# Kernel tuning notes

Measured on AMD Instinct MI355X. Metric: run time of the kernel, lower is better.

## Reference

```python
import jax, jax.numpy as jnp
import numpy as np

B, T, G, M, D = 8, 2048, 2, 1024, 256
ALPHA = -1.0      # config['dist_to_logits_alpha']
TAU = 2.0         # curr_temp = max_temp at init
EPS = 1e-10


def setup_inputs() -> dict:
    key = jax.random.key(0)
    k1, k2, k3 = jax.random.split(key, 3)
    x = jax.random.normal(k1, (B, T, G * D), dtype=jnp.float32)
    # nn.init.uniform_(embedding, -0.999, 0.999)
    embedding = jax.random.uniform(k2, (G, M, D), dtype=jnp.float32, minval=-0.999, maxval=0.999)
    # uniform noise for gumbel sampling, clipped away from {0,1}
    gumbel_u = jax.random.uniform(k3, (B * T, G, M), dtype=jnp.float32, minval=1e-6, maxval=1.0 - 1e-6)
    return {"x": x, "embedding": embedding, "gumbel_u": gumbel_u}


def reference(x, embedding, gumbel_u):
    b, t, c = x.shape
    g, m, d = embedding.shape
    xf = x.reshape(-1, g, d)                                  # [N, G, D]

    sq_e = jnp.sum(embedding ** 2, axis=-1)                   # [G, M]
    sq_x = jnp.sum(xf ** 2, axis=-1, keepdims=True)           # [N, G, 1]
    cross = jnp.einsum('ngd,gmd->ngm', xf, embedding)         # [N, G, M]
    logits = ALPHA * (sq_e[None] + sq_x - 2.0 * cross)        # [N, G, M]

    # hard-assignment code perplexity
    hard_x = jax.nn.one_hot(jnp.argmax(logits, axis=-1), m, dtype=logits.dtype)
    hard_probs = hard_x.mean(axis=0)                          # [G, M]
    code_perplexity = -jnp.sum(hard_probs * jnp.log2(hard_probs + EPS), axis=-1)

    # soft-assignment prob perplexity
    avg_probs = jax.nn.softmax(logits, axis=-1).mean(axis=0)  # [G, M]
    prob_perplexity = -jnp.sum(avg_probs * jnp.log2(avg_probs + EPS), axis=-1)

    # gumbel-softmax (hard=True, straight-through)
    gumbels = -jnp.log(-jnp.log(gumbel_u))
    y_soft = jax.nn.softmax((logits + gumbels) / TAU, axis=-1)
    idx = jnp.argmax(y_soft, axis=-1)                         # [N, G]
    y_hard = jax.nn.one_hot(idx, m, dtype=y_soft.dtype)
    st = y_hard + y_soft - jax.lax.stop_gradient(y_soft)      # straight-through one-hot

    # weighted sum over the codebook (avoids [N, G, M, D] blowup of the original)
    quantized = jnp.einsum('ngm,gmd->ngd', st, embedding).reshape(b, t, c)

    quantization_inds = idx.reshape(b, t, g).astype(jnp.int32)
    # use_vq_loss=True: F.mse_loss(x, quantized.detach())
    commitment_loss = jnp.mean((x - jax.lax.stop_gradient(quantized)) ** 2)

    return quantized, code_perplexity, prob_perplexity, quantization_inds, commitment_loss
```

## Files before the change

### kernel.cpp

```cpp
#include <hip/hip_runtime.h>
#include <math.h>

#define NTOT 16384
#define GG 2
#define MM 1024
#define DD 256

#define OFF_Q  ((size_t)0)
#define OFF_CP ((size_t)8388608)
#define OFF_PP ((size_t)8388610)
#define OFF_I  ((size_t)8388612)
#define OFF_L  ((size_t)8421380)

#define SHIFT 40.0f
#define REFINE_GAP 0.03f

typedef __attribute__((ext_vector_type(8))) short bf16x8;
typedef __attribute__((ext_vector_type(4))) float f32x4;
typedef unsigned short u16;
typedef unsigned int u32;

__device__ inline float wave_sum_f(float v) {
#pragma unroll
  for (int o = 32; o > 0; o >>= 1) v += __shfl_xor(v, o);
  return v;
}
__device__ inline u16 f2bf(float f) {
  u32 u = __float_as_uint(f);
  return (u16)((u + 0x7fffu + ((u >> 16) & 1u)) >> 16);
}
__device__ inline float bf2f(u16 h) {
  return __uint_as_float(((u32)h) << 16);
}
__device__ inline void async16(const void* g, void* l) {
  __builtin_amdgcn_global_load_lds(
      (const __attribute__((address_space(1))) u32*)g,
      (__attribute__((address_space(3))) u32*)l, 16, 0, 0);
}
__device__ inline float neg_log_acc(float u) {
  float t1 = 1.0f - u;
  float se = t1 * (1.f + t1 * (0.5f + t1 * (0.33333334f + t1 * 0.25f)));
  float fl = -__logf(u);
  return (t1 < 0.015625f) ? se : fl;
}

#define WS_INVZ   32768
#define WS_EHSW   163840
#define WS_ELSW   1212416
#define WS_EST    2260992
#define WS_NEED3  (2260992ull + 2ull * MM * (size_t)NTOT * GG)

__global__ void vq_init2(const float* __restrict__ emb, float* __restrict__ sq_e,
                         float* __restrict__ avg, int* __restrict__ hist,
                         double* __restrict__ loss, u16* __restrict__ eh,
                         u16* __restrict__ el, int do_split) {
  const int row = blockIdx.x * 4 + (threadIdx.x >> 6);
  const int lane = threadIdx.x & 63;
  float4 e4 = *(const float4*)&emb[(size_t)row * DD + lane * 4];
  float s = e4.x * e4.x + e4.y * e4.y + e4.z * e4.z + e4.w * e4.w;
  s = wave_sum_f(s);
  if (do_split) {
    ushort4 h, l;
    h.x = f2bf(e4.x); l.x = f2bf(e4.x - bf2f(h.x));
    h.y = f2bf(e4.y); l.y = f2bf(e4.y - bf2f(h.y));
    h.z = f2bf(e4.z); l.z = f2bf(e4.z - bf2f(h.z));
    h.w = f2bf(e4.w); l.w = f2bf(e4.w - bf2f(h.w));
    *(ushort4*)&eh[(size_t)row * DD + lane * 4] = h;
    *(ushort4*)&el[(size_t)row * DD + lane * 4] = l;
  }
  if (lane == 0) sq_e[row] = s;
  if (blockIdx.x == 0) {
    for (int i = threadIdx.x; i < GG * MM; i += 256) { avg[i] = 0.f; hist[i] = 0; }
    if (threadIdx.x == 0) *loss = 0.0;
  }
}

__global__ void vq_init_swz(const float* __restrict__ emb, u16* __restrict__ eh_sw,
                            u16* __restrict__ el_sw) {
  int tid = blockIdx.x * 256 + threadIdx.x;
  int g = tid >> 15, rem = tid & 32767;
  int col = rem >> 5, kc = rem & 31;
  const float* src = emb + ((size_t)(g * MM + col)) * DD + kc * 8;
  float4 fa = *(const float4*)src;
  float4 fb = *(const float4*)(src + 4);
  float f[8] = {fa.x, fa.y, fa.z, fa.w, fb.x, fb.y, fb.z, fb.w};
  u16 hi[8], lo[8];
#pragma unroll
  for (int j = 0; j < 8; ++j) {
    hi[j] = f2bf(f[j]);
    lo[j] = f2bf(f[j] - bf2f(hi[j]));
  }
  int ct = col >> 6, cg = (col >> 4) & 3, l15 = col & 15;
  int ks = kc >> 2, quad = kc & 3;
  size_t chunk = ((((size_t)g * 16 + ct) * 8 + ks) * 4 + cg) * 64 + quad * 16 + l15;
  ushort4* dh = (ushort4*)(eh_sw + chunk * 8);
  ushort4* dl = (ushort4*)(el_sw + chunk * 8);
  dh[0] = make_ushort4(hi[0], hi[1], hi[2], hi[3]);
  dh[1] = make_ushort4(hi[4], hi[5], hi[6], hi[7]);
  dl[0] = make_ushort4(lo[0], lo[1], lo[2], lo[3]);
  dl[1] = make_ushort4(lo[4], lo[5], lo[6], lo[7]);
}

__global__ __launch_bounds__(512, 2) void vq_main3(
    const float* __restrict__ x, const float* __restrict__ emb,
    const float* __restrict__ gum, const float* __restrict__ sq_e,
    const u16* __restrict__ eh_sw, const u16* __restrict__ el_sw,
    float* __restrict__ out, u16* __restrict__ est, float* __restrict__ invZ_ws,
    int* __restrict__ hist, double* __restrict__ loss) {
  __shared__ u16 bt[2][32768];
  __shared__ int fidx_lds[128];

  const int g = blockIdx.y;
  const int n0 = blockIdx.x * 128;
  const int t = threadIdx.x;
  const int wave = t >> 6, lane = t & 63;
  const int quad = lane >> 4, l15 = lane & 15;
  const int nw = n0 + wave * 16;

  float* xs = (float*)&bt[0][0];
  {
    const float* xb = x + (size_t)nw * (GG * DD) + (size_t)g * DD;
#pragma unroll 4
    for (int j = 0; j < 16; ++j) {
      float4 v = *(const float4*)(xb + (size_t)j * (GG * DD) + lane * 4);
      *(float4*)&xs[wave * 4096 + j * 256 + ((lane ^ (j & 7)) << 2)] = v;
    }
  }

  bf16x8 ah[8], al[8];
#pragma unroll
  for (int ks = 0; ks < 8; ++ks) {
    int row = l15;
    int c0 = ks * 8 + quad * 2;
    const float* base = &xs[wave * 4096 + row * 256];
    float4 f0 = *(const float4*)&base[((c0 ^ (row & 7)) << 2)];
    float4 f1 = *(const float4*)&base[(((c0 + 1) ^ (row & 7)) << 2)];
    float f[8] = {f0.x, f0.y, f0.z, f0.w, f1.x, f1.y, f1.z, f1.w};
#pragma unroll
    for (int j = 0; j < 8; ++j) {
      u16 h = f2bf(f[j]);
      ah[ks][j] = (short)h;
      al[ks][j] = (short)f2bf(f[j] - bf2f(h));
    }
  }
  __syncthreads();

  const u16* sgh = eh_sw + (size_t)g * 16 * 16384;
  const u16* sgl = el_sw + (size_t)g * 16 * 16384;

  auto stage = [&](int ct, int buf) {
    const u16* sh = sgh + (size_t)ct * 16384;
    const u16* sl = sgl + (size_t)ct * 16384;
    u16* dh = &bt[buf][0];
    u16* dl = &bt[buf][16384];
#pragma unroll
    for (int j = 0; j < 4; ++j) {
      int slot = j * 8 + wave;
      async16(sh + slot * 512 + lane * 8, dh + slot * 512);
      async16(sl + slot * 512 + lane * 8, dl + slot * 512);
    }
  };

  float Zl[4], hv[4], z1[4], z2[4];
  int hid[4], i1[4], i2[4];
#pragma unroll
  for (int i = 0; i < 4; ++i) {
    Zl[i] = 0.f; hv[i] = -INFINITY; z1[i] = -INFINITY; z2[i] = -INFINITY;
    hid[i] = 0; i1[i] = 0; i2[i] = 0;
  }

  stage(0, 0);

  const float* gumb = gum + ((size_t)(nw + quad * 4) * GG + g) * MM + l15;
  const float* sqb = sq_e + g * MM + l15;
  float gA[4], gB[4], sqA, sqB;
#pragma unroll
  for (int r = 0; r < 4; ++r) gA[r] = gumb[(size_t)r * (GG * MM)];
#pragma unroll
  for (int r = 0; r < 4; ++r) gB[r] = gumb[(size_t)r * (GG * MM) + 16];
  sqA = sqb[0];
  sqB = sqb[16];

#pragma unroll 1
  for (int ct = 0; ct < 16; ++ct) {
    __syncthreads();
    if (ct < 15) stage(ct + 1, (ct + 1) & 1);
    const u16* bh_p = &bt[ct & 1][0];
    const u16* bl_p = &bt[ct & 1][16384];
#pragma unroll 1
    for (int cg = 0; cg < 4; ++cg) {
      const int s = ct * 4 + cg;
      const int colG = s * 16 + l15;
      int sn = s + 2; if (sn > 63) sn = 63;
      float gN[4], sqN;
#pragma unroll
      for (int r = 0; r < 4; ++r) gN[r] = gumb[(size_t)r * (GG * MM) + sn * 16];
      sqN = sqb[sn * 16];

      f32x4 c0 = {0,0,0,0}, c1 = {0,0,0,0}, c2 = {0,0,0,0};
#pragma unroll
      for (int ks = 0; ks < 8; ++ks) {
        int off = ((ks * 4 + cg) * 64 + lane) * 8;
        bf16x8 bh = *(const bf16x8*)(bh_p + off);
        bf16x8 bl = *(const bf16x8*)(bl_p + off);
        c0 = __builtin_amdgcn_mfma_f32_16x16x32_bf16(ah[ks], bh, c0, 0, 0, 0);
        c1 = __builtin_amdgcn_mfma_f32_16x16x32_bf16(ah[ks], bl, c1, 0, 0, 0);
        c2 = __builtin_amdgcn_mfma_f32_16x16x32_bf16(al[ks], bh, c2, 0, 0, 0);
      }
      float ev[4];
#pragma unroll
      for (int r = 0; r < 4; ++r) {
        float lp = 2.f * (c0[r] + c1[r] + c2[r]) - sqA + SHIFT;
        float e = __expf(fminf(lp, 80.f));
        Zl[r] += e;
        ev[r] = e;
        if (lp > hv[r]) { hv[r] = lp; hid[r] = colG; }
        float zz = lp - __logf(neg_log_acc(gA[r]));
        if (zz > z1[r]) {
          z2[r] = z1[r]; i2[r] = i1[r];
          z1[r] = zz; i1[r] = colG;
        } else if (zz > z2[r]) {
          z2[r] = zz; i2[r] = colG;
        }
      }
      u32 p01, p23;
      asm("v_cvt_pk_bf16_f32 %0, %1, %2" : "=v"(p01) : "v"(ev[0]), "v"(ev[1]));
      asm("v_cvt_pk_bf16_f32 %0, %1, %2" : "=v"(p23) : "v"(ev[2]), "v"(ev[3]));
      uint2 pk2 = make_uint2(p01, p23);
      *(uint2*)&est[((size_t)(g * MM + colG) << 14) + nw + quad * 4] = pk2;
#pragma unroll
      for (int r = 0; r < 4; ++r) { gA[r] = gB[r]; gB[r] = gN[r]; }
      sqA = sqB; sqB = sqN;
    }
  }

#pragma unroll 1
  for (int r = 0; r < 4; ++r) {
    const int row = wave * 16 + quad * 4 + r;
    const int n = n0 + row;
    float Zr = Zl[r], hvr = hv[r];
    int hir = hid[r];
    float v1 = z1[r], v2 = z2[r];
    int j1 = i1[r], j2 = i2[r];
#pragma unroll
    for (int o = 1; o <= 8; o <<= 1) {
      Zr += __shfl_xor(Zr, o);
      float ohv = __shfl_xor(hvr, o); int ohi = __shfl_xor(hir, o);
      if (ohv > hvr || (ohv == hvr && ohi < hir)) { hvr = ohv; hir = ohi; }
      float w1 = __shfl_xor(v1, o), w2 = __shfl_xor(v2, o);
      int k1 = __shfl_xor(j1, o), k2 = __shfl_xor(j2, o);
      if (w1 > v1 || (w1 == v1 && k1 < j1)) {
        if (v1 > w2 || (v1 == w2 && j1 < k2)) { v2 = v1; j2 = j1; }
        else { v2 = w2; j2 = k2; }
        v1 = w1; j1 = k1;
      } else if (w1 > v2 || (w1 == v2 && k1 < j2)) { v2 = w1; j2 = k1; }
    }
    int fidx = j1;
    if (v1 - v2 < REFINE_GAP) {
      const float* xrow = x + (size_t)n * (GG * DD) + (size_t)g * DD;
      const float* eA = emb + ((size_t)g * MM + j1) * DD;
      const float* eB = emb + ((size_t)g * MM + j2) * DD;
      double dA = 0, sA = 0, dB = 0, sB = 0;
#pragma unroll
      for (int k = 0; k < 16; ++k) {
        int d = l15 * 16 + k;
        double xv = (double)xrow[d];
        double ea = (double)eA[d], eb = (double)eB[d];
        dA += xv * ea; sA += ea * ea;
        dB += xv * eb; sB += eb * eb;
      }
#pragma unroll
      for (int o = 1; o <= 8; o <<= 1) {
        dA += __shfl_xor(dA, o); sA += __shfl_xor(sA, o);
        dB += __shfl_xor(dB, o); sB += __shfl_xor(sB, o);
      }
      double uA = (double)gum[((size_t)n * GG + g) * MM + j1];
      double uB = (double)gum[((size_t)n * GG + g) * MM + j2];
      double zA = 2.0 * dA - sA - log(-log(uA));
      double zB = 2.0 * dB - sB - log(-log(uB));
      if (zB > zA || (zB == zA && j2 < j1)) fidx = j2;
    }
    if (l15 == 0) {
      out[OFF_I + (size_t)n * GG + g] = (float)fidx;
      atomicAdd(&hist[g * MM + hir], 1);
      invZ_ws[g * NTOT + n] = 1.f / Zr;
      fidx_lds[row] = fidx;
    }
  }
  __syncthreads();

  {
    float ls = 0.f;
#pragma unroll
    for (int j = 0; j < 16; ++j) {
      int idx = j * 512 + t;
      int row = idx >> 6, f4 = idx & 63;
      int n = n0 + row, fi = fidx_lds[row];
      float4 e4 = *(const float4*)&emb[((size_t)g * MM + fi) * DD + f4 * 4];
      float4 x4 = *(const float4*)&x[(size_t)n * (GG * DD) + (size_t)g * DD + f4 * 4];
      *(float4*)&out[OFF_Q + (size_t)n * (GG * DD) + (size_t)g * DD + f4 * 4] = e4;
      float dx = x4.x - e4.x, dy = x4.y - e4.y, dz = x4.z - e4.z, dw = x4.w - e4.w;
      ls += dx * dx + dy * dy + dz * dz + dw * dw;
    }
    ls = wave_sum_f(ls);
    if (lane == 0) atomicAdd(loss, (double)ls);
  }
}

__global__ void vq_avg(const u16* __restrict__ est, const float* __restrict__ invZ,
                       float* __restrict__ avg) {
  int wid = blockIdx.x;
  int t = threadIdx.x;
  const u16* base = est + ((size_t)wid << 14);
  const float* zp = invZ + ((wid >> 10) << 14);
  float acc = 0.f;
#pragma unroll
  for (int it = 0; it < 8; ++it) {
    int n = it * 2048 + t * 8;
    uint4 e = *(const uint4*)(base + n);
    float4 z0 = *(const float4*)(zp + n);
    float4 z1 = *(const float4*)(zp + n + 4);
    acc += bf2f((u16)(e.x & 0xffff)) * z0.x + bf2f((u16)(e.x >> 16)) * z0.y +
           bf2f((u16)(e.y & 0xffff)) * z0.z + bf2f((u16)(e.y >> 16)) * z0.w +
           bf2f((u16)(e.z & 0xffff)) * z1.x + bf2f((u16)(e.z >> 16)) * z1.y +
           bf2f((u16)(e.w & 0xffff)) * z1.z + bf2f((u16)(e.w >> 16)) * z1.w;
  }
  acc = wave_sum_f(acc);
  __shared__ float sw[4];
  if ((t & 63) == 0) sw[t >> 6] = acc;
  __syncthreads();
  if (t == 0) avg[wid] = sw[0] + sw[1] + sw[2] + sw[3];
}

__global__ void vq_fin(const float* __restrict__ avg, const int* __restrict__ hist,
                       const double* __restrict__ loss, float* __restrict__ out) {
  int g = blockIdx.x, t = threadIdx.x;
  float cp = 0.f, pp = 0.f;
  for (int m = t; m < MM; m += 256) {
    float hp = (float)hist[g * MM + m] * (1.f / 16384.f);
    cp += hp * log2f(hp + 1e-10f);
    float ap = avg[g * MM + m] * (1.f / 16384.f);
    pp += ap * log2f(ap + 1e-10f);
  }
  cp = wave_sum_f(cp);
  pp = wave_sum_f(pp);
  __shared__ float sc[4], sp[4];
  int wave = t >> 6, lane = t & 63;
  if (lane == 0) { sc[wave] = cp; sp[wave] = pp; }
  __syncthreads();
  if (t == 0) {
    out[OFF_CP + g] = -(sc[0] + sc[1] + sc[2] + sc[3]);
    out[OFF_PP + g] = -(sp[0] + sp[1] + sp[2] + sp[3]);
    if (g == 0) out[OFF_L] = (float)(*loss * (1.0 / 8388608.0));
  }
}

__global__ __launch_bounds__(256, 3) void vq_main_fast(
    const float* __restrict__ x, const float* __restrict__ emb,
    const float* __restrict__ gum, const float* __restrict__ sq_e,
    const u16* __restrict__ eh, const u16* __restrict__ el,
    float* __restrict__ out, float* __restrict__ avg,
    int* __restrict__ hist, double* __restrict__ loss) {
  __shared__ u16 est_lds[4][16][264];
  __shared__ float colsum[MM];
  __shared__ float red[16][4][8];
  __shared__ float fin_invZ[16];
  __shared__ int fin_idx[16];

  const int g = blockIdx.y;
  const int n0 = blockIdx.x * 16;
  const int t = threadIdx.x;
  const int wave = t >> 6, lane = t & 63;
  const int quad = lane >> 4, l15 = lane & 15;
  const int wm0 = wave * 256;

  for (int i = t; i < MM; i += 256) colsum[i] = 0.f;

  bf16x8 ah[8], al[8];
  {
    const float* xr = x + (size_t)(n0 + l15) * (GG * DD) + (size_t)g * DD + quad * 8;
#pragma unroll
    for (int ks = 0; ks < 8; ++ks) {
      float4 fa = *(const float4*)(xr + ks * 32);
      float4 fb = *(const float4*)(xr + ks * 32 + 4);
      float f[8] = {fa.x, fa.y, fa.z, fa.w, fb.x, fb.y, fb.z, fb.w};
#pragma unroll
      for (int j = 0; j < 8; ++j) {
        u16 h = f2bf(f[j]);
        ah[ks][j] = (short)h;
        al[ks][j] = (short)f2bf(f[j] - bf2f(h));
      }
    }
  }
  const u16* ehb = eh + ((size_t)g * MM + wm0 + l15) * DD + quad * 8;
  const u16* elb = el + ((size_t)g * MM + wm0 + l15) * DD + quad * 8;
  const float* sqb = sq_e + g * MM + wm0 + l15;

  float Z[4] = {0.f, 0.f, 0.f, 0.f};
  float hv[4] = {-INFINITY, -INFINITY, -INFINITY, -INFINITY};
  int hid[4] = {0, 0, 0, 0};
  float z1[4] = {-INFINITY, -INFINITY, -INFINITY, -INFINITY};
  float z2[4] = {-INFINITY, -INFINITY, -INFINITY, -INFINITY};
  int i1[4] = {0, 0, 0, 0}, i2[4] = {0, 0, 0, 0};

#pragma unroll 2
  for (int tt = 0; tt < 16; ++tt) {
    float sqv = sqb[tt * 16];
    float gv[4];
#pragma unroll
    for (int r = 0; r < 4; ++r)
      gv[r] = gum[((size_t)(n0 + quad * 4 + r) * GG + g) * MM + wm0 + tt * 16 + l15];
    f32x4 a0 = {0,0,0,0}, a1 = {0,0,0,0}, a2 = {0,0,0,0};
#pragma unroll
    for (int ks = 0; ks < 8; ++ks) {
      bf16x8 bh = *(const bf16x8*)(ehb + (size_t)tt * 16 * DD + ks * 32);
      bf16x8 bl = *(const bf16x8*)(elb + (size_t)tt * 16 * DD + ks * 32);
      a0 = __builtin_amdgcn_mfma_f32_16x16x32_bf16(ah[ks], bh, a0, 0, 0, 0);
      a1 = __builtin_amdgcn_mfma_f32_16x16x32_bf16(ah[ks], bl, a1, 0, 0, 0);
      a2 = __builtin_amdgcn_mfma_f32_16x16x32_bf16(al[ks], bh, a2, 0, 0, 0);
    }
    const int colL = tt * 16 + l15;
    const int colG = wm0 + colL;
#pragma unroll
    for (int r = 0; r < 4; ++r) {
      float lp = 2.f * (a0[r] + a1[r] + a2[r]) - sqv + SHIFT;
      float ev = expf(fminf(lp, 80.f));
      Z[r] += ev;
      est_lds[wave][quad * 4 + r][colL] = f2bf(ev);
      if (lp > hv[r]) { hv[r] = lp; hid[r] = colG; }
      float zz = lp - logf(-logf(gv[r]));
      if (zz > z1[r]) { z2[r] = z1[r]; i2[r] = i1[r]; z1[r] = zz; i1[r] = colG; }
      else if (zz > z2[r]) { z2[r] = zz; i2[r] = colG; }
    }
  }
#pragma unroll
  for (int r = 0; r < 4; ++r) {
    float Zr = Z[r], hvr = hv[r];
    int hir = hid[r];
    float v1 = z1[r], v2 = z2[r];
    int j1 = i1[r], j2 = i2[r];
#pragma unroll
    for (int o = 1; o <= 8; o <<= 1) {
      Zr += __shfl_xor(Zr, o);
      float ohv = __shfl_xor(hvr, o); int ohi = __shfl_xor(hir, o);
      if (ohv > hvr || (ohv == hvr && ohi < hir)) { hvr = ohv; hir = ohi; }
      float w1 = __shfl_xor(v1, o), w2 = __shfl_xor(v2, o);
      int k1 = __shfl_xor(j1, o), k2 = __shfl_xor(j2, o);
      if (w1 > v1 || (w1 == v1 && k1 < j1)) {
        if (v1 > w2 || (v1 == w2 && j1 < k2)) { v2 = v1; j2 = j1; }
        else { v2 = w2; j2 = k2; }
        v1 = w1; j1 = k1;
      } else if (w1 > v2 || (w1 == v2 && k1 < j2)) { v2 = w1; j2 = k1; }
    }
    if (l15 == 0) {
      float* rp = red[quad * 4 + r][wave];
      rp[0] = Zr; rp[1] = hvr; rp[2] = __int_as_float(hir);
      rp[3] = v1; rp[4] = __int_as_float(j1);
      rp[5] = v2; rp[6] = __int_as_float(j2);
    }
  }
  __syncthreads();
  if (t < 16) {
    const int row = t, n = n0 + row;
    float Zf = 0.f, hvf = -INFINITY; int hif = 0;
    float v1 = -INFINITY, v2 = -INFINITY; int j1 = 0, j2 = 0;
    for (int w = 0; w < 4; ++w) {
      const float* rp = red[row][w];
      Zf += rp[0];
      float ohv = rp[1]; int ohi = __float_as_int(rp[2]);
      if (ohv > hvf || (ohv == hvf && ohi < hif)) { hvf = ohv; hif = ohi; }
      float w1 = rp[3], w2 = rp[5];
      int k1 = __float_as_int(rp[4]), k2 = __float_as_int(rp[6]);
      if (w1 > v1 || (w1 == v1 && k1 < j1)) {
        if (v1 > w2 || (v1 == w2 && j1 < k2)) { v2 = v1; j2 = j1; }
        else { v2 = w2; j2 = k2; }
        v1 = w1; j1 = k1;
      } else if (w1 > v2 || (w1 == v2 && k1 < j2)) { v2 = w1; j2 = k1; }
    }
    int fidx = j1;
    if (v1 - v2 < REFINE_GAP) {
      const float* xrow = x + (size_t)n * (GG * DD) + (size_t)g * DD;
      const float* eA = emb + ((size_t)g * MM + j1) * DD;
      const float* eB = emb + ((size_t)g * MM + j2) * DD;
      double dA = 0, sA = 0, dB = 0, sB = 0;
      for (int d = 0; d < DD; ++d) {
        double xv = xrow[d], ea = eA[d], eb = eB[d];
        dA += xv * ea; sA += ea * ea;
        dB += xv * eb; sB += eb * eb;
      }
      double uA = gum[((size_t)n * GG + g) * MM + j1];
      double uB = gum[((size_t)n * GG + g) * MM + j2];
      double zA = 2.0 * dA - sA - log(-log(uA));
      double zB = 2.0 * dB - sB - log(-log(uB));
      if (zB > zA || (zB == zA && j2 < j1)) fidx = j2;
    }
    out[OFF_I + (size_t)n * GG + g] = (float)fidx;
    atomicAdd(&hist[g * MM + hif], 1);
    fin_invZ[row] = 1.f / Zf;
    fin_idx[row] = fidx;
  }
  __syncthreads();
  {
    const int row = t >> 4, c = (t & 15) * 16;
    const int n = n0 + row, fidx = fin_idx[row];
    const float* er = emb + ((size_t)g * MM + fidx) * DD + c;
    const float* xq = x + (size_t)n * (GG * DD) + (size_t)g * DD + c;
    float* op = out + OFF_Q + (size_t)n * (GG * DD) + (size_t)g * DD + c;
    float ls = 0.f;
#pragma unroll
    for (int j = 0; j < 4; ++j) {
      float4 e4 = *(const float4*)(er + j * 4);
      float4 x4 = *(const float4*)(xq + j * 4);
      *(float4*)(op + j * 4) = e4;
      float dx = x4.x - e4.x, dy = x4.y - e4.y, dz = x4.z - e4.z, dw = x4.w - e4.w;
      ls += dx * dx + dy * dy + dz * dz + dw * dw;
    }
    ls = wave_sum_f(ls);
    if (lane == 0) atomicAdd(loss, (double)ls);
  }
  float iZ[4];
#pragma unroll
  for (int r = 0; r < 4; ++r) iZ[r] = fin_invZ[quad * 4 + r];
#pragma unroll 1
  for (int tt = 0; tt < 16; ++tt) {
    float v = 0.f;
#pragma unroll
    for (int r = 0; r < 4; ++r)
      v += bf2f(est_lds[wave][quad * 4 + r][tt * 16 + l15]) * iZ[r];
    v += __shfl_xor(v, 16);
    v += __shfl_xor(v, 32);
    if (lane < 16) colsum[wm0 + tt * 16 + lane] += v;
  }
  __syncthreads();
  for (int i = t; i < MM; i += 256) atomicAdd(&avg[g * MM + i], colsum[i]);
}

extern "C" void kernel_launch(void* const* d_in, const int* in_sizes, int n_in,
                              void* d_out, int out_size, void* d_ws, size_t ws_size,
                              hipStream_t stream) {
  const float* x = (const float*)d_in[0];
  const float* emb = (const float*)d_in[1];
  const float* gum = (const float*)d_in[2];
  float* out = (float*)d_out;

  float* sq_e = (float*)d_ws;
  float* avg = (float*)((char*)d_ws + 8192);
  int* hist = (int*)((char*)d_ws + 16384);
  double* loss = (double*)((char*)d_ws + 24576);

  if (ws_size >= WS_NEED3) {
    float* invZ = (float*)((char*)d_ws + WS_INVZ);
    u16* eh_sw = (u16*)((char*)d_ws + WS_EHSW);
    u16* el_sw = (u16*)((char*)d_ws + WS_ELSW);
    u16* est = (u16*)((char*)d_ws + WS_EST);
    vq_init2<<<512, 256, 0, stream>>>(emb, sq_e, avg, hist, loss, eh_sw, el_sw, 0);
    vq_init_swz<<<256, 256, 0, stream>>>(emb, eh_sw, el_sw);
    vq_main3<<<dim3(NTOT / 128, GG), 512, 0, stream>>>(
        x, emb, gum, sq_e, eh_sw, el_sw, out, est, invZ, hist, loss);
    vq_avg<<<2048, 256, 0, stream>>>(est, invZ, avg);
    vq_fin<<<GG, 256, 0, stream>>>(avg, hist, loss, out);
  } else {
    u16* eh = (u16*)((char*)d_ws + 32768);
    u16* el = eh + (size_t)GG * MM * DD;
    vq_init2<<<512, 256, 0, stream>>>(emb, sq_e, avg, hist, loss, eh, el, 1);
    vq_main_fast<<<dim3(NTOT / 16, GG), 256, 0, stream>>>(
        x, emb, gum, sq_e, eh, el, out, avg, hist, loss);
    vq_fin<<<GG, 256, 0, stream>>>(avg, hist, loss, out);
  }
}
```

Before: 345.1 us.

## Split codebook columns across two wave halves with 1024-thread blocks and LDS merge

Doubles the block to 16 waves. Each group of 8 waves handles the same 128 rows but half of every 64-column tile, so per-wave MFMA and softmax work per tile halves. The partial row statistics (sum of exp, hard argmax, top-2 gumbel) from the second half are merged through a new LDS buffer before the refinement and output stage. The aim is more in-flight waves to hide latency, at the cost of an extra barrier, an LDS merge, and 'launch_bounds(1024,4)' register limits that may cause spilling given the bf16 A fragments held in registers.

```diff
diff --git a/kernel.cpp b/kernel.cpp
--- a/kernel.cpp
+++ b/kernel.cpp
@@ -101,46 +101,51 @@
   dl[1] = make_ushort4(lo[4], lo[5], lo[6], lo[7]);
 }
 
-__global__ __launch_bounds__(512, 2) void vq_main3(
+__global__ __launch_bounds__(1024, 4) void vq_main3(
     const float* __restrict__ x, const float* __restrict__ emb,
     const float* __restrict__ gum, const float* __restrict__ sq_e,
     const u16* __restrict__ eh_sw, const u16* __restrict__ el_sw,
     float* __restrict__ out, u16* __restrict__ est, float* __restrict__ invZ_ws,
     int* __restrict__ hist, double* __restrict__ loss) {
   __shared__ u16 bt[2][32768];
+  __shared__ float mrg[128][8];
   __shared__ int fidx_lds[128];
 
   const int g = blockIdx.y;
   const int n0 = blockIdx.x * 128;
   const int t = threadIdx.x;
   const int wave = t >> 6, lane = t & 63;
+  const int ws = wave & 7, h = wave >> 3;
   const int quad = lane >> 4, l15 = lane & 15;
-  const int nw = n0 + wave * 16;
+  const int nw = n0 + ws * 16;
 
   float* xs = (float*)&bt[0][0];
   {
-    const float* xb = x + (size_t)nw * (GG * DD) + (size_t)g * DD;
-#pragma unroll 4
-    for (int j = 0; j < 16; ++j) {
-      float4 v = *(const float4*)(xb + (size_t)j * (GG * DD) + lane * 4);
-      *(float4*)&xs[wave * 4096 + j * 256 + ((lane ^ (j & 7)) << 2)] = v;
-    }
-  }
+    const float* xb = x + (size_t)n0 * (GG * DD) + (size_t)g * DD;
+#pragma unroll
+    for (int j = 0; j < 8; ++j) {
+      int idx = j * 1024 + t;
+      int row = idx >> 6, ch = idx & 63;
+      float4 v = *(const float4*)(xb + (size_t)row * (GG * DD) + ch * 4);
+      *(float4*)&xs[row * 256 + ((ch ^ (row & 7)) << 2)] = v;
+    }
+  }
+  __syncthreads();
 
   bf16x8 ah[8], al[8];
 #pragma unroll
   for (int ks = 0; ks < 8; ++ks) {
-    int row = l15;
+    int row = ws * 16 + l15;
     int c0 = ks * 8 + quad * 2;
-    const float* base = &xs[wave * 4096 + row * 256];
+    const float* base = &xs[row * 256];
     float4 f0 = *(const float4*)&base[((c0 ^ (row & 7)) << 2)];
     float4 f1 = *(const float4*)&base[(((c0 + 1) ^ (row & 7)) << 2)];
     float f[8] = {f0.x, f0.y, f0.z, f0.w, f1.x, f1.y, f1.z, f1.w};
 #pragma unroll
     for (int j = 0; j < 8; ++j) {
-      u16 h = f2bf(f[j]);
-      ah[ks][j] = (short)h;
-      al[ks][j] = (short)f2bf(f[j] - bf2f(h));
+      u16 hh = f2bf(f[j]);
+      ah[ks][j] = (short)hh;
+      al[ks][j] = (short)f2bf(f[j] - bf2f(hh));
     }
   }
   __syncthreads();
@@ -154,8 +159,8 @@
     u16* dh = &bt[buf][0];
     u16* dl = &bt[buf][16384];
 #pragma unroll
-    for (int j = 0; j < 4; ++j) {
-      int slot = j * 8 + wave;
+    for (int j = 0; j < 2; ++j) {
+      int slot = j * 16 + wave;
       async16(sh + slot * 512 + lane * 8, dh + slot * 512);
       async16(sl + slot * 512 + lane * 8, dl + slot * 512);
     }
@@ -171,8 +176,9 @@
 
   stage(0, 0);
 
-  const float* gumb = gum + ((size_t)(nw + quad * 4) * GG + g) * MM + l15;
-  const float* sqb = sq_e + g * MM + l15;
+  const float* gumb =
+      gum + ((size_t)(nw + quad * 4) * GG + g) * MM + h * 32 + l15;
+  const float* sqb = sq_e + g * MM + h * 32 + l15;
   float gA[4], gB[4], sqA, sqB;
 #pragma unroll
   for (int r = 0; r < 4; ++r) gA[r] = gumb[(size_t)r * (GG * MM)];
@@ -188,14 +194,16 @@
     const u16* bh_p = &bt[ct & 1][0];
     const u16* bl_p = &bt[ct & 1][16384];
 #pragma unroll 1
-    for (int cg = 0; cg < 4; ++cg) {
-      const int s = ct * 4 + cg;
-      const int colG = s * 16 + l15;
-      int sn = s + 2; if (sn > 63) sn = 63;
+    for (int j = 0; j < 2; ++j) {
+      const int cg = h * 2 + j;
+      const int sw = ct * 2 + j;
+      const int colG = ct * 64 + cg * 16 + l15;
+      int sn = sw + 2; if (sn > 31) sn = 31;
+      const int offN = (sn >> 1) * 64 + (sn & 1) * 16;
       float gN[4], sqN;
 #pragma unroll
-      for (int r = 0; r < 4; ++r) gN[r] = gumb[(size_t)r * (GG * MM) + sn * 16];
-      sqN = sqb[sn * 16];
+      for (int r = 0; r < 4; ++r) gN[r] = gumb[(size_t)r * (GG * MM) + offN];
+      sqN = sqb[offN];
 
       f32x4 c0 = {0,0,0,0}, c1 = {0,0,0,0}, c2 = {0,0,0,0};
 #pragma unroll
@@ -234,10 +242,10 @@
     }
   }
 
+  float Zr4[4], hv4[4], v14[4], v24[4];
+  int hi4[4], j14[4], j24[4];
 #pragma unroll 1
   for (int r = 0; r < 4; ++r) {
-    const int row = wave * 16 + quad * 4 + r;
-    const int n = n0 + row;
     float Zr = Zl[r], hvr = hv[r];
     int hir = hid[r];
     float v1 = z1[r], v2 = z2[r];
@@ -255,36 +263,70 @@
         v1 = w1; j1 = k1;
       } else if (w1 > v2 || (w1 == v2 && k1 < j2)) { v2 = w1; j2 = k1; }
     }
-    int fidx = j1;
-    if (v1 - v2 < REFINE_GAP) {
-      const float* xrow = x + (size_t)n * (GG * DD) + (size_t)g * DD;
-      const float* eA = emb + ((size_t)g * MM + j1) * DD;
-      const float* eB = emb + ((size_t)g * MM + j2) * DD;
-      double dA = 0, sA = 0, dB = 0, sB = 0;
-#pragma unroll
-      for (int k = 0; k < 16; ++k) {
-        int d = l15 * 16 + k;
-        double xv = (double)xrow[d];
-        double ea = (double)eA[d], eb = (double)eB[d];
-        dA += xv * ea; sA += ea * ea;
-        dB += xv * eb; sB += eb * eb;
+    Zr4[r] = Zr; hv4[r] = hvr; hi4[r] = hir;
+    v14[r] = v1; j14[r] = j1; v24[r] = v2; j24[r] = j2;
+    if (h == 1 && l15 == 0) {
+      float* rp = mrg[ws * 16 + quad * 4 + r];
+      rp[0] = Zr; rp[1] = hvr; rp[2] = __int_as_float(hir);
+      rp[3] = v1; rp[4] = __int_as_float(j1);
+      rp[5] = v2; rp[6] = __int_as_float(j2);
+    }
+  }
+  __syncthreads();
+
+  if (h == 0) {
+#pragma unroll 1
+    for (int r = 0; r < 4; ++r) {
+      const int row = ws * 16 + quad * 4 + r;
+      const int n = n0 + row;
+      float Zr = Zr4[r], hvr = hv4[r];
+      int hir = hi4[r];
+      float v1 = v14[r], v2 = v24[r];
+      int j1 = j14[r], j2 = j24[r];
+      const float* rp = mrg[row];
+      Zr += rp[0];
+      {
+        float ohv = rp[1]; int ohi = __float_as_int(rp[2]);
+        if (ohv > hvr || (ohv == hvr && ohi < hir)) { hvr = ohv; hir = ohi; }
+        float w1 = rp[3], w2 = rp[5];
+        int k1 = __float_as_int(rp[4]), k2 = __float_as_int(rp[6]);
+        if (w1 > v1 || (w1 == v1 && k1 < j1)) {
+          if (v1 > w2 || (v1 == w2 && j1 < k2)) { v2 = v1; j2 = j1; }
+          else { v2 = w2; j2 = k2; }
+          v1 = w1; j1 = k1;
+        } else if (w1 > v2 || (w1 == v2 && k1 < j2)) { v2 = w1; j2 = k1; }
       }
-#pragma unroll
-      for (int o = 1; o <= 8; o <<= 1) {
-        dA += __shfl_xor(dA, o); sA += __shfl_xor(sA, o);
-        dB += __shfl_xor(dB, o); sB += __shfl_xor(sB, o);
+      int fidx = j1;
+      if (v1 - v2 < REFINE_GAP) {
+        const float* xrow = x + (size_t)n * (GG * DD) + (size_t)g * DD;
+        const float* eA = emb + ((size_t)g * MM + j1) * DD;
+        const float* eB = emb + ((size_t)g * MM + j2) * DD;
+        double dA = 0, sA = 0, dB = 0, sB = 0;
+#pragma unroll
+        for (int k = 0; k < 16; ++k) {
+          int d = l15 * 16 + k;
+          double xv = (double)xrow[d];
+          double ea = (double)eA[d], eb = (double)eB[d];
+          dA += xv * ea; sA += ea * ea;
+          dB += xv * eb; sB += eb * eb;
+        }
+#pragma unroll
+        for (int o = 1; o <= 8; o <<= 1) {
+          dA += __shfl_xor(dA, o); sA += __shfl_xor(sA, o);
+          dB += __shfl_xor(dB, o); sB += __shfl_xor(sB, o);
+        }
+        double uA = (double)gum[((size_t)n * GG + g) * MM + j1];
+        double uB = (double)gum[((size_t)n * GG + g) * MM + j2];
+        double zA = 2.0 * dA - sA - log(-log(uA));
+        double zB = 2.0 * dB - sB - log(-log(uB));
+        if (zB > zA || (zB == zA && j2 < j1)) fidx = j2;
       }
-      double uA = (double)gum[((size_t)n * GG + g) * MM + j1];
-      double uB = (double)gum[((size_t)n * GG + g) * MM + j2];
-      double zA = 2.0 * dA - sA - log(-log(uA));
-      double zB = 2.0 * dB - sB - log(-log(uB));
-      if (zB > zA || (zB == zA && j2 < j1)) fidx = j2;
-    }
-    if (l15 == 0) {
-      out[OFF_I + (size_t)n * GG + g] = (float)fidx;
-      atomicAdd(&hist[g * MM + hir], 1);
-      invZ_ws[g * NTOT + n] = 1.f / Zr;
-      fidx_lds[row] = fidx;
+      if (l15 == 0) {
+        out[OFF_I + (size_t)n * GG + g] = (float)fidx;
+        atomicAdd(&hist[g * MM + hir], 1);
+        invZ_ws[g * NTOT + n] = 1.f / Zr;
+        fidx_lds[row] = fidx;
+      }
     }
   }
   __syncthreads();
@@ -292,8 +334,8 @@
   {
     float ls = 0.f;
 #pragma unroll
-    for (int j = 0; j < 16; ++j) {
-      int idx = j * 512 + t;
+    for (int j = 0; j < 8; ++j) {
+      int idx = j * 1024 + t;
       int row = idx >> 6, f4 = idx & 63;
       int n = n0 + row, fi = fidx_lds[row];
       float4 e4 = *(const float4*)&emb[((size_t)g * MM + fi) * DD + f4 * 4];
@@ -555,7 +597,7 @@
     u16* est = (u16*)((char*)d_ws + WS_EST);
     vq_init2<<<512, 256, 0, stream>>>(emb, sq_e, avg, hist, loss, eh_sw, el_sw, 0);
     vq_init_swz<<<256, 256, 0, stream>>>(emb, eh_sw, el_sw);
-    vq_main3<<<dim3(NTOT / 128, GG), 512, 0, stream>>>(
+    vq_main3<<<dim3(NTOT / 128, GG), 1024, 0, stream>>>(
         x, emb, gum, sq_e, eh_sw, el_sw, out, est, invZ, hist, loss);
     vq_avg<<<2048, 256, 0, stream>>>(est, invZ, avg);
     vq_fin<<<GG, 256, 0, stream>>>(avg, hist, loss, out);
```

Measured after the change: 669.4 us. +94.0%, slower.
